# Kernel optimization log

Measured on AMD Instinct MI355X. Metric: run time of the kernel, lower is better.

The kernel has to match this reference:

```python
import jax, jax.numpy as jnp
import numpy as np
from jax import lax


def _make_grid():
    # Faithful replication of the torch buffer construction in __init__.
    r = np.arange(-128, 128) * np.pi / 256.0
    X, Y = np.meshgrid(r, r, indexing='ij')            # torch.meshgrid default 'ij'
    grid = np.tile(np.stack([X, Y], 0), (16, 1, 1))    # [32,256,256] channels x,y,x,y,...
    scales = 2.0 ** np.repeat(np.arange(16) / 2.0, 2)  # [32]: f0,f0,f1,f1,...
    grid = np.sin(grid * scales[:, None, None])
    return jnp.asarray(grid.reshape(32, 256 * 256).T, dtype=jnp.float32)  # [65536,32]

IMG_GRID = _make_grid()


def _conv_lrelu(x, w, b, padding, groups):
    y = lax.conv_general_dilated(x, w, (1, 1), padding,
                                 feature_group_count=groups,
                                 dimension_numbers=('NCHW', 'OIHW', 'NCHW'))
    return jax.nn.leaky_relu(y + b[None, :, None, None])


def _wn_linear(x, v, g, b):
    # nn.utils.weight_norm(Linear): w = g * v / ||v||  (norm over input dim, per output row)
    w = v * (g / jnp.linalg.norm(v, axis=1))[:, None]
    return x @ w.T + b


def _mem_stack(x, vf, gf, bf, vg, gg, bg):
    # memcnn AdditiveCoupling: x1,x2 = chunk(x,2); y1 = x1 + Fm(x2); y2 = x2 + Gm(y1)
    def step(h, p):
        pvf, pgf, pbf, pvg, pgg, pbg = p
        h1, h2 = jnp.split(h, 2, axis=-1)
        y1 = h1 + jax.nn.leaky_relu(_wn_linear(h2, pvf, pgf, pbf))
        y2 = h2 + jax.nn.leaky_relu(_wn_linear(y1, pvg, pgg, pbg))
        return jnp.concatenate([y1, y2], axis=-1), None
    h, _ = lax.scan(step, x, (vf, gf, bf, vg, gg, bg))
    return h


def _forward(feature, cw1, cb1, cw2, cb2, cw3, cb3, cw4, cb4, cw5, cb5,
             w1, b1, m1_vf, m1_gf, m1_bf, m1_vg, m1_gg, m1_bg,
             w2, b2, m2_vf, m2_gf, m2_bf, m2_vg, m2_gg, m2_bg, w3, b3):
    B = feature.shape[0]
    h = _conv_lrelu(feature, cw1, cb1, 'SAME', 4)
    h = _conv_lrelu(h, cw2, cb2, 'SAME', 3)
    h = _conv_lrelu(h, cw3, cb3, 'SAME', 2)
    h = _conv_lrelu(h, cw4, cb4, 'VALID', 3)
    h = _conv_lrelu(h, cw5, cb5, 'VALID', 1)   # [B,128,4,4]
    feat = h.reshape(B, -1)                    # [B,2048]
    N = IMG_GRID.shape[0]                      # 65536 coords, fully vectorized (no python chunk loop)
    grid_b = jnp.broadcast_to(IMG_GRID[None], (B, N, 32))
    x = jnp.concatenate([grid_b, jnp.broadcast_to(feat[:, None, :], (B, N, feat.shape[1]))], -1)
    mid = jax.nn.leaky_relu(x @ w1.T + b1)     # [B,N,1024]
    mid = _mem_stack(mid, m1_vf, m1_gf, m1_bf, m1_vg, m1_gg, m1_bg)
    h2 = jax.nn.leaky_relu(jnp.concatenate([grid_b, mid], -1) @ w2.T + b2)  # [B,N,512]
    h2 = _mem_stack(h2, m2_vf, m2_gf, m2_bf, m2_vg, m2_gg, m2_bg)
    rgb = jax.nn.sigmoid(h2 @ w3.T + b3)       # [B,N,3]
    img = rgb.transpose(0, 2, 1).reshape(B, 3, 256, 256)
    return img * 1.1 - 0.05


def setup_inputs() -> dict:
    key = jax.random.key(0)
    ks = iter(jax.random.split(key, 48))
    def nrm(shape, s=0.02):
        return jax.random.normal(next(ks), shape, jnp.float32) * s
    def gpar(shape):
        return jax.random.uniform(next(ks), shape, jnp.float32, 0.5, 1.0)
    inp = {}
    inp['feature'] = jax.random.normal(next(ks), (1, 1792, 8, 8), jnp.float32)
    inp['cw1'] = nrm((768, 448, 3, 3)); inp['cb1'] = nrm((768,), 0.01)   # groups=4: 1792/4=448
    inp['cw2'] = nrm((768, 256, 3, 3)); inp['cb2'] = nrm((768,), 0.01)   # groups=3
    inp['cw3'] = nrm((768, 384, 3, 3)); inp['cb3'] = nrm((768,), 0.01)   # groups=2
    inp['cw4'] = nrm((768, 256, 3, 3)); inp['cb4'] = nrm((768,), 0.01)   # groups=3, valid
    inp['cw5'] = nrm((128, 768, 3, 3)); inp['cb5'] = nrm((128,), 0.01)   # groups=1, valid
    inp['w1'] = nrm((1024, 2080)); inp['b1'] = nrm((1024,), 0.01)
    inp['m1_vf'] = nrm((8, 512, 512), 1.0); inp['m1_gf'] = gpar((8, 512)); inp['m1_bf'] = nrm((8, 512), 0.01)
    inp['m1_vg'] = nrm((8, 512, 512), 1.0); inp['m1_gg'] = gpar((8, 512)); inp['m1_bg'] = nrm((8, 512), 0.01)
    inp['w2'] = nrm((512, 1056)); inp['b2'] = nrm((512,), 0.01)
    inp['m2_vf'] = nrm((8, 256, 256), 1.0); inp['m2_gf'] = gpar((8, 256)); inp['m2_bf'] = nrm((8, 256), 0.01)
    inp['m2_vg'] = nrm((8, 256, 256), 1.0); inp['m2_gg'] = gpar((8, 256)); inp['m2_bg'] = nrm((8, 256), 0.01)
    inp['w3'] = nrm((3, 512)); inp['b3'] = nrm((3,), 0.01)
    return inp


def reference(feature, cw1, cb1, cw2, cb2, cw3, cb3, cw4, cb4, cw5, cb5,
              w1, b1, m1_vf, m1_gf, m1_bf, m1_vg, m1_gg, m1_bg,
              w2, b2, m2_vf, m2_gf, m2_bf, m2_vg, m2_gg, m2_bg, w3, b3):
    return _forward(feature, cw1, cb1, cw2, cb2, cw3, cb3, cw4, cb4, cw5, cb5,
                    w1, b1, m1_vf, m1_gf, m1_bf, m1_vg, m1_gg, m1_bg,
                    w2, b2, m2_vf, m2_gf, m2_bf, m2_vg, m2_gg, m2_bg, w3, b3)
```

## Files before the change

### kernel.cpp

```cpp
#include <hip/hip_runtime.h>
#include <cmath>

#define LRELU(x) fmaxf((x), 0.01f * (x))

typedef __attribute__((ext_vector_type(8))) short short8;
typedef __attribute__((ext_vector_type(4))) float f32x4;
typedef __attribute__((ext_vector_type(2))) unsigned uint2v;

constexpr int RS = 1032;

__device__ __forceinline__ unsigned short f2bf(float f) {
    return __builtin_bit_cast(unsigned short, (__bf16)f);
}
__device__ __forceinline__ unsigned pk2(unsigned short a, unsigned short b) {
    return (unsigned)a | ((unsigned)b << 16);
}
__device__ __forceinline__ uint2v cvt4(f32x4 v) {
    uint2v r;
    r[0] = pk2(f2bf(v[0]), f2bf(v[1]));
    r[1] = pk2(f2bf(v[2]), f2bf(v[3]));
    return r;
}
__device__ __forceinline__ f32x4 unpk4(uint2v p) {
    f32x4 r;
    r[0] = __uint_as_float(p[0] << 16);
    r[1] = __uint_as_float(p[0] & 0xffff0000u);
    r[2] = __uint_as_float(p[1] << 16);
    r[3] = __uint_as_float(p[1] & 0xffff0000u);
    return r;
}
__device__ __forceinline__ f32x4 lrelu4(f32x4 v) {
    return __builtin_elementwise_max(v, 0.01f * v);
}

__global__ void sgrid_kernel(float* __restrict__ sg) {
    int idx = blockIdx.x * blockDim.x + threadIdx.x;
    if (idx >= 256 * 32) return;
    int t = idx >> 5, c = idx & 31;
    double r = (double)(t - 128) * 3.14159265358979323846 / 256.0;
    double scale = exp2(0.5 * (double)(c >> 1));
    sg[idx] = (float)sin(r * scale);
}

__global__ __launch_bounds__(256) void conv_part(
    const float* __restrict__ x, const float* __restrict__ w,
    float* __restrict__ y, int Cin_g, int Cout_g, int Hin, int pad) {
    __shared__ float wsh[64 * 9];
    __shared__ float red[256];
    int oc = blockIdx.x, ch = blockIdx.y;
    int Hout = pad ? Hin : Hin - 2;
    int t = threadIdx.x;
    int ic0 = ch * 64;
    int nic = min(64, Cin_g - ic0);
    const float* wb = w + ((size_t)oc * Cin_g + ic0) * 9;
    for (int i = t; i < nic * 9; i += 256) wsh[i] = wb[i];
    __syncthreads();
    int p = t & 63, sub = t >> 6;
    int oy = p / Hout, ox = p % Hout;
    int g = oc / Cout_g;
    const float* xb = x + ((size_t)g * Cin_g + ic0) * Hin * Hin;
    bool valid = p < Hout * Hout;
    float acc = 0.f;
    if (valid) {
        for (int ic = sub; ic < nic; ic += 4) {
            const float* xc = xb + (size_t)ic * Hin * Hin;
            const float* wc = wsh + ic * 9;
            #pragma unroll
            for (int ky = 0; ky < 3; ++ky) {
                int iy = oy + ky - pad;
                if (iy < 0 || iy >= Hin) continue;
                #pragma unroll
                for (int kx = 0; kx < 3; ++kx) {
                    int ix = ox + kx - pad;
                    if (ix < 0 || ix >= Hin) continue;
                    acc = fmaf(xc[iy * Hin + ix], wc[ky * 3 + kx], acc);
                }
            }
        }
    }
    red[t] = acc;
    __syncthreads();
    if (t < 64 && valid)
        atomicAdd(&y[(size_t)oc * Hout * Hout + p],
                  red[t] + red[t + 64] + red[t + 128] + red[t + 192]);
}

__global__ void conv_finalize(float* __restrict__ y, const float* __restrict__ bias,
                              int HH, int n) {
    int i = blockIdx.x * 256 + threadIdx.x;
    if (i >= n) return;
    float v = y[i] + bias[i / HH];
    y[i] = LRELU(v);
}

__global__ void feat_c1_kernel(const float* __restrict__ feat, const float* __restrict__ w1,
                               const float* __restrict__ b1, float* __restrict__ c1) {
    int o = (blockIdx.x * blockDim.x + threadIdx.x) >> 6;
    int lane = threadIdx.x & 63;
    if (o >= 1024) return;
    const float* wr = w1 + (size_t)o * 2080 + 32;
    float sum = 0.f;
    for (int k = lane; k < 2048; k += 64) sum += feat[k] * wr[k];
    #pragma unroll
    for (int off = 32; off; off >>= 1) sum += __shfl_xor(sum, off);
    if (lane == 0) c1[o] = sum + b1[o];
}

__global__ __launch_bounds__(256) void wn_all(
    const float* __restrict__ v1f, const float* __restrict__ g1f, float* __restrict__ s1f,
    const float* __restrict__ v1g, const float* __restrict__ g1g, float* __restrict__ s1g,
    const float* __restrict__ v2f, const float* __restrict__ g2f, float* __restrict__ s2f,
    const float* __restrict__ v2g, const float* __restrict__ g2g, float* __restrict__ s2g) {
    __shared__ float red[256];
    int b = blockIdx.x, t = threadIdx.x;
    const float* v; const float* g; float* s; int K, r;
    if (b < 4096)       { v = v1f; g = g1f; s = s1f; K = 512; r = b; }
    else if (b < 8192)  { v = v1g; g = g1g; s = s1g; K = 512; r = b - 4096; }
    else if (b < 10240) { v = v2f; g = g2f; s = s2f; K = 256; r = b - 8192; }
    else                { v = v2g; g = g2g; s = s2g; K = 256; r = b - 10240; }
    const float* vr = v + (size_t)r * K;
    float sum = 0.f;
    for (int k = t; k < K; k += 256) { float x = vr[k]; sum = fmaf(x, x, sum); }
    red[t] = sum;
    __syncthreads();
    for (int o = 128; o; o >>= 1) {
        if (t < o) red[t] += red[t + o];
        __syncthreads();
    }
    if (t == 0) s[r] = g[r] / sqrtf(red[0]);
}

__device__ __forceinline__ void repack_one(const float* __restrict__ v, unsigned short* __restrict__ dst,
                                           int N, int NT, int KC, int ldk, int koff, size_t fi) {
    int W = N / (NT * 16);
    int l = (int)(fi & 63);
    size_t r = fi >> 6;
    int kc = r % KC; r /= KC;
    int nt = r % NT; r /= NT;
    int w  = r % W;  r /= W;
    int t  = (int)r;
    int n = w * NT * 16 + nt * 16 + (l & 15);
    int k = kc * 32 + (l >> 4) * 8;
    const float* src = v + ((size_t)t * N + n) * ldk + koff + k;
    unsigned short* d = dst + fi * 8;
    #pragma unroll
    for (int e = 0; e < 8; ++e) d[e] = f2bf(src[e]);
}

__global__ void repack_all(const float* __restrict__ m1vf, const float* __restrict__ m1vg,
                           const float* __restrict__ m2vf, const float* __restrict__ m2vg,
                           const float* __restrict__ w2,
                           unsigned short* __restrict__ p1f, unsigned short* __restrict__ p1g,
                           unsigned short* __restrict__ p2f, unsigned short* __restrict__ p2g,
                           unsigned short* __restrict__ pw2) {
    size_t fi = (size_t)blockIdx.x * 256 + threadIdx.x;
    const size_t n1 = 262144, n2 = 65536;
    if (fi < n1)                repack_one(m1vf, p1f, 512, 4, 16, 512, 0, fi);
    else if (fi < 2 * n1)       repack_one(m1vg, p1g, 512, 4, 16, 512, 0, fi - n1);
    else if (fi < 2 * n1 + n2)  repack_one(m2vf, p2f, 256, 2, 8, 256, 0, fi - 2 * n1);
    else if (fi < 2 * n1 + 2 * n2) repack_one(m2vg, p2g, 256, 2, 8, 256, 0, fi - 2 * n1 - n2);
    else                        repack_one(w2, pw2, 512, 4, 32, 1056, 32, fi - 2 * n1 - 2 * n2);
}

__global__ void pq_kernel(const float* __restrict__ sg, const float* __restrict__ w1,
                          const float* __restrict__ c1, const float* __restrict__ w2,
                          float* __restrict__ Px, float* __restrict__ Py,
                          float* __restrict__ Qx, float* __restrict__ Qy) {
    int idx = blockIdx.x * 256 + threadIdx.x;
    if (idx < 256 * 1024) {
        int t = idx >> 10, o = idx & 1023;
        const float* wr = w1 + (size_t)o * 2080;
        const float* sr = sg + t * 32;
        float px = 0.f, py = 0.f;
        #pragma unroll
        for (int k = 0; k < 16; ++k) {
            px = fmaf(sr[2 * k], wr[2 * k], px);
            py = fmaf(sr[2 * k + 1], wr[2 * k + 1], py);
        }
        Px[idx] = px + c1[o];
        Py[idx] = py;
    } else {
        int j = idx - 256 * 1024;
        int t = j >> 9, o = j & 511;
        const float* wr = w2 + (size_t)o * 1056;
        const float* sr = sg + t * 32;
        float qx = 0.f, qy = 0.f;
        #pragma unroll
        for (int k = 0; k < 16; ++k) {
            qx = fmaf(sr[2 * k], wr[2 * k], qx);
            qy = fmaf(sr[2 * k + 1], wr[2 * k + 1], qy);
        }
        Qx[j] = qx;
        Qy[j] = qy;
    }
}

__device__ __forceinline__ void step1(unsigned short* sm, int w, int l, int l15, int lq,
                                      int srcb, int dstb,
                                      const unsigned short* __restrict__ Bp,
                                      const float* __restrict__ sc,
                                      const float* __restrict__ bi,
                                      uint2v* lo_half) {
    f32x4 acc[4][4] = {};
    const unsigned short* wb = Bp + (size_t)w * (4 * 16 * 512) + (size_t)l * 8;
    const unsigned short* abase = sm + (size_t)l15 * RS + srcb + lq * 8;
    short8 b0[4], b1[4];
    #pragma unroll
    for (int nt = 0; nt < 4; ++nt) b0[nt] = *(const short8*)(wb + (size_t)(nt * 16 + 0) * 512);
    #pragma unroll
    for (int nt = 0; nt < 4; ++nt) b1[nt] = *(const short8*)(wb + (size_t)(nt * 16 + 1) * 512);
    #pragma unroll
    for (int kc = 0; kc < 16; ++kc) {
        short8 bn[4];
        if (kc < 14) {
            #pragma unroll
            for (int nt = 0; nt < 4; ++nt)
                bn[nt] = *(const short8*)(wb + (size_t)(nt * 16 + kc + 2) * 512);
        }
        short8 af[4];
        #pragma unroll
        for (int mt = 0; mt < 4; ++mt)
            af[mt] = *(const short8*)(abase + (size_t)(mt * 16) * RS + kc * 32);
        #pragma unroll
        for (int mt = 0; mt < 4; ++mt)
            #pragma unroll
            for (int nt = 0; nt < 4; ++nt)
                acc[mt][nt] = __builtin_amdgcn_mfma_f32_16x16x32_bf16(b0[nt], af[mt], acc[mt][nt], 0, 0, 0);
        #pragma unroll
        for (int nt = 0; nt < 4; ++nt) { b0[nt] = b1[nt]; b1[nt] = bn[nt]; }
    }
    #pragma unroll
    for (int nt = 0; nt < 4; ++nt) {
        int nb = w * 64 + nt * 16 + lq * 4;
        f32x4 s4 = *(const f32x4*)(sc + nb);
        f32x4 bb = *(const f32x4*)(bi + nb);
        #pragma unroll
        for (int mt = 0; mt < 4; ++mt) {
            int row = mt * 16 + l15;
            size_t hidx = (size_t)row * RS + dstb + nb;
            uint2v hold = *(uint2v*)(sm + hidx);
            f32x4 v = lrelu4(acc[mt][nt] * s4 + bb);
            v += unpk4(hold) + unpk4(lo_half[mt * 4 + nt]);
            uint2v hnew = cvt4(v);
            *(uint2v*)(sm + hidx) = hnew;
            lo_half[mt * 4 + nt] = cvt4(v - unpk4(hnew));
        }
    }
}

__device__ __forceinline__ void step2(unsigned short* sm, int w, int l, int l15, int lq,
                                      int srcb, int dstb,
                                      const unsigned short* __restrict__ Bp,
                                      const float* __restrict__ sc,
                                      const float* __restrict__ bi) {
    f32x4 acc[4][2] = {};
    const unsigned short* wb = Bp + (size_t)w * (2 * 8 * 512) + (size_t)l * 8;
    const unsigned short* abase = sm + (size_t)l15 * RS + srcb + lq * 8;
    short8 b0[2], b1[2];
    #pragma unroll
    for (int nt = 0; nt < 2; ++nt) b0[nt] = *(const short8*)(wb + (size_t)(nt * 8 + 0) * 512);
    #pragma unroll
    for (int nt = 0; nt < 2; ++nt) b1[nt] = *(const short8*)(wb + (size_t)(nt * 8 + 1) * 512);
    #pragma unroll
    for (int kc = 0; kc < 8; ++kc) {
        short8 bn[2];
        if (kc < 6) {
            #pragma unroll
            for (int nt = 0; nt < 2; ++nt)
                bn[nt] = *(const short8*)(wb + (size_t)(nt * 8 + kc + 2) * 512);
        }
        short8 af[4];
        #pragma unroll
        for (int mt = 0; mt < 4; ++mt)
            af[mt] = *(const short8*)(abase + (size_t)(mt * 16) * RS + kc * 32);
        #pragma unroll
        for (int mt = 0; mt < 4; ++mt)
            #pragma unroll
            for (int nt = 0; nt < 2; ++nt)
                acc[mt][nt] = __builtin_amdgcn_mfma_f32_16x16x32_bf16(b0[nt], af[mt], acc[mt][nt], 0, 0, 0);
        #pragma unroll
        for (int nt = 0; nt < 2; ++nt) { b0[nt] = b1[nt]; b1[nt] = bn[nt]; }
    }
    #pragma unroll
    for (int nt = 0; nt < 2; ++nt) {
        int nb = w * 32 + nt * 16 + lq * 4;
        f32x4 s4 = *(const f32x4*)(sc + nb);
        f32x4 bb = *(const f32x4*)(bi + nb);
        #pragma unroll
        for (int mt = 0; mt < 4; ++mt) {
            int row = mt * 16 + l15;
            size_t hidx = (size_t)row * RS + dstb + nb;
            uint2v hold = *(uint2v*)(sm + hidx);
            uint2v lold = *(uint2v*)(sm + hidx + 512);
            f32x4 v = lrelu4(acc[mt][nt] * s4 + bb);
            v += unpk4(hold) + unpk4(lold);
            uint2v hnew = cvt4(v);
            *(uint2v*)(sm + hidx) = hnew;
            *(uint2v*)(sm + hidx + 512) = cvt4(v - unpk4(hnew));
        }
    }
}

__global__ __launch_bounds__(512, 2) void fused_mlp(
    const float* __restrict__ Px, const float* __restrict__ Py,
    const float* __restrict__ Qx, const float* __restrict__ Qy,
    const unsigned short* __restrict__ m1f, const float* __restrict__ s1f, const float* __restrict__ bf1,
    const unsigned short* __restrict__ m1g, const float* __restrict__ s1g, const float* __restrict__ bg1,
    const unsigned short* __restrict__ w2m, const float* __restrict__ b2,
    const unsigned short* __restrict__ m2f, const float* __restrict__ s2f, const float* __restrict__ bf2_,
    const unsigned short* __restrict__ m2g, const float* __restrict__ s2g, const float* __restrict__ bg2_,
    const float* __restrict__ w3, const float* __restrict__ b3,
    float* __restrict__ out) {
    extern __shared__ unsigned short sm[];
    int tid = threadIdx.x;
    int w = tid >> 6, l = tid & 63;
    int l15 = l & 15, lq = l >> 4;
    int n0 = blockIdx.x * 64;
    int i = n0 >> 8, jb = n0 & 255;

    uint2v lo_pk[32];

    #pragma unroll
    for (int h = 0; h < 2; ++h) {
        #pragma unroll
        for (int nt = 0; nt < 4; ++nt) {
            int nb = h * 512 + w * 64 + nt * 16 + lq * 4;
            f32x4 px4 = *(const f32x4*)(Px + (size_t)i * 1024 + nb);
            #pragma unroll
            for (int mt = 0; mt < 4; ++mt) {
                int row = mt * 16 + l15;
                f32x4 py4 = *(const f32x4*)(Py + (size_t)(jb + row) * 1024 + nb);
                f32x4 v = lrelu4(px4 + py4);
                uint2v hv = cvt4(v);
                *(uint2v*)(sm + (size_t)row * RS + nb) = hv;
                lo_pk[h * 16 + mt * 4 + nt] = cvt4(v - unpk4(hv));
            }
        }
    }
    __syncthreads();

    for (int t = 0; t < 8; ++t) {
        step1(sm, w, l, l15, lq, 512, 0, m1f + (size_t)t * 512 * 512, s1f + t * 512, bf1 + t * 512, lo_pk);
        __syncthreads();
        step1(sm, w, l, l15, lq, 0, 512, m1g + (size_t)t * 512 * 512, s1g + t * 512, bg1 + t * 512, lo_pk + 16);
        __syncthreads();
    }

    {
        f32x4 acc[4][4] = {};
        const unsigned short* wb = w2m + (size_t)w * (4 * 32 * 512) + (size_t)l * 8;
        const unsigned short* abase = sm + (size_t)l15 * RS + lq * 8;
        short8 b0[4], b1[4];
        #pragma unroll
        for (int nt = 0; nt < 4; ++nt) b0[nt] = *(const short8*)(wb + (size_t)(nt * 32 + 0) * 512);
        #pragma unroll
        for (int nt = 0; nt < 4; ++nt) b1[nt] = *(const short8*)(wb + (size_t)(nt * 32 + 1) * 512);
        #pragma unroll
        for (int kc = 0; kc < 32; ++kc) {
            short8 bn[4];
            if (kc < 30) {
                #pragma unroll
                for (int nt = 0; nt < 4; ++nt)
                    bn[nt] = *(const short8*)(wb + (size_t)(nt * 32 + kc + 2) * 512);
            }
            short8 af[4];
            #pragma unroll
            for (int mt = 0; mt < 4; ++mt)
                af[mt] = *(const short8*)(abase + (size_t)(mt * 16) * RS + kc * 32);
            #pragma unroll
            for (int mt = 0; mt < 4; ++mt)
                #pragma unroll
                for (int nt = 0; nt < 4; ++nt)
                    acc[mt][nt] = __builtin_amdgcn_mfma_f32_16x16x32_bf16(b0[nt], af[mt], acc[mt][nt], 0, 0, 0);
            #pragma unroll
            for (int nt = 0; nt < 4; ++nt) { b0[nt] = b1[nt]; b1[nt] = bn[nt]; }
        }
        __syncthreads();
        #pragma unroll
        for (int nt = 0; nt < 4; ++nt) {
            int nb = w * 64 + nt * 16 + lq * 4;
            f32x4 qx4 = *(const f32x4*)(Qx + (size_t)i * 512 + nb);
            f32x4 b24 = *(const f32x4*)(b2 + nb);
            #pragma unroll
            for (int mt = 0; mt < 4; ++mt) {
                int row = mt * 16 + l15;
                f32x4 qy4 = *(const f32x4*)(Qy + (size_t)(jb + row) * 512 + nb);
                f32x4 v = lrelu4(acc[mt][nt] + qx4 + qy4 + b24);
                uint2v hv = cvt4(v);
                size_t hidx = (size_t)row * RS + nb;
                *(uint2v*)(sm + hidx) = hv;
                *(uint2v*)(sm + hidx + 512) = cvt4(v - unpk4(hv));
            }
        }
    }
    __syncthreads();

    for (int t = 0; t < 8; ++t) {
        step2(sm, w, l, l15, lq, 256, 0, m2f + (size_t)t * 256 * 256, s2f + t * 256, bf2_ + t * 256);
        __syncthreads();
        step2(sm, w, l, l15, lq, 0, 256, m2g + (size_t)t * 256 * 256, s2g + t * 256, bg2_ + t * 256);
        __syncthreads();
    }

    #pragma unroll
    for (int rr = 0; rr < 8; ++rr) {
        int row = w * 8 + rr;
        float s0 = 0.f, s1 = 0.f, s2 = 0.f;
        #pragma unroll
        for (int it = 0; it < 8; ++it) {
            int k = it * 64 + l;
            size_t hidx = (size_t)row * RS + k;
            float hv = __uint_as_float((unsigned)sm[hidx] << 16) +
                       __uint_as_float((unsigned)sm[hidx + 512] << 16);
            s0 = fmaf(hv, w3[k], s0);
            s1 = fmaf(hv, w3[512 + k], s1);
            s2 = fmaf(hv, w3[1024 + k], s2);
        }
        #pragma unroll
        for (int off = 32; off; off >>= 1) {
            s0 += __shfl_xor(s0, off);
            s1 += __shfl_xor(s1, off);
            s2 += __shfl_xor(s2, off);
        }
        if (l == 0) {
            float v[3] = {s0 + b3[0], s1 + b3[1], s2 + b3[2]};
            #pragma unroll
            for (int c = 0; c < 3; ++c) {
                float sg = 1.0f / (1.0f + expf(-v[c]));
                out[(size_t)c * 65536 + n0 + row] = 1.1f * sg - 0.05f;
            }
        }
    }
}

extern "C" void kernel_launch(void* const* d_in, const int* in_sizes, int n_in,
                              void* d_out, int out_size, void* d_ws, size_t ws_size,
                              hipStream_t stream) {
    const float* feature = (const float*)d_in[0];
    const float* cw1 = (const float*)d_in[1];  const float* cb1 = (const float*)d_in[2];
    const float* cw2 = (const float*)d_in[3];  const float* cb2 = (const float*)d_in[4];
    const float* cw3 = (const float*)d_in[5];  const float* cb3 = (const float*)d_in[6];
    const float* cw4 = (const float*)d_in[7];  const float* cb4 = (const float*)d_in[8];
    const float* cw5 = (const float*)d_in[9];  const float* cb5 = (const float*)d_in[10];
    const float* w1  = (const float*)d_in[11]; const float* b1  = (const float*)d_in[12];
    const float* m1_vf = (const float*)d_in[13]; const float* m1_gf = (const float*)d_in[14];
    const float* m1_bf = (const float*)d_in[15];
    const float* m1_vg = (const float*)d_in[16]; const float* m1_gg = (const float*)d_in[17];
    const float* m1_bg = (const float*)d_in[18];
    const float* w2  = (const float*)d_in[19]; const float* b2  = (const float*)d_in[20];
    const float* m2_vf = (const float*)d_in[21]; const float* m2_gf = (const float*)d_in[22];
    const float* m2_bf = (const float*)d_in[23];
    const float* m2_vg = (const float*)d_in[24]; const float* m2_gg = (const float*)d_in[25];
    const float* m2_bg = (const float*)d_in[26];
    const float* w3  = (const float*)d_in[27]; const float* b3  = (const float*)d_in[28];
    float* out = (float*)d_out;

    float* ws = (float*)d_ws;
    size_t off = 0;
    float* sgrid   = ws + off; off += 256 * 32;
    float* cbA     = ws + off; off += 768 * 64;
    float* cbB     = ws + off; off += 768 * 64;
    float* cbC     = ws + off; off += 768 * 64;
    float* cbD     = ws + off; off += 768 * 36;
    float* featbuf = ws + off; off += 2048;
    size_t convN   = 768 * 64 * 3 + 768 * 36 + 2048;
    float* c1      = ws + off; off += 1024;
    float* s1f     = ws + off; off += 8 * 512;
    float* s1g     = ws + off; off += 8 * 512;
    float* s2f     = ws + off; off += 8 * 256;
    float* s2g     = ws + off; off += 8 * 256;
    float* Px      = ws + off; off += 256 * 1024;
    float* Py      = ws + off; off += 256 * 1024;
    float* Qx      = ws + off; off += 256 * 512;
    float* Qy      = ws + off; off += 256 * 512;
    unsigned short* m1f_p = (unsigned short*)(ws + off); off += (size_t)8 * 512 * 512 / 2;
    unsigned short* m1g_p = (unsigned short*)(ws + off); off += (size_t)8 * 512 * 512 / 2;
    unsigned short* m2f_p = (unsigned short*)(ws + off); off += (size_t)8 * 256 * 256 / 2;
    unsigned short* m2g_p = (unsigned short*)(ws + off); off += (size_t)8 * 256 * 256 / 2;
    unsigned short* w2m_p = (unsigned short*)(ws + off); off += (size_t)512 * 1024 / 2;

    sgrid_kernel<<<32, 256, 0, stream>>>(sgrid);
    wn_all<<<12288, 256, 0, stream>>>(m1_vf, m1_gf, s1f, m1_vg, m1_gg, s1g,
                                      m2_vf, m2_gf, s2f, m2_vg, m2_gg, s2g);
    repack_all<<<2816, 256, 0, stream>>>(m1_vf, m1_vg, m2_vf, m2_vg, w2,
                                         m1f_p, m1g_p, m2f_p, m2g_p, w2m_p);

    hipMemsetAsync(cbA, 0, convN * sizeof(float), stream);
    conv_part<<<dim3(768, 7), 256, 0, stream>>>(feature, cw1, cbA, 448, 192, 8, 1);
    conv_finalize<<<(768 * 64) / 256, 256, 0, stream>>>(cbA, cb1, 64, 768 * 64);
    conv_part<<<dim3(768, 4), 256, 0, stream>>>(cbA, cw2, cbB, 256, 256, 8, 1);
    conv_finalize<<<(768 * 64) / 256, 256, 0, stream>>>(cbB, cb2, 64, 768 * 64);
    conv_part<<<dim3(768, 6), 256, 0, stream>>>(cbB, cw3, cbC, 384, 384, 8, 1);
    conv_finalize<<<(768 * 64) / 256, 256, 0, stream>>>(cbC, cb3, 64, 768 * 64);
    conv_part<<<dim3(768, 4), 256, 0, stream>>>(cbC, cw4, cbD, 256, 256, 8, 0);
    conv_finalize<<<(768 * 36 + 255) / 256, 256, 0, stream>>>(cbD, cb4, 36, 768 * 36);
    conv_part<<<dim3(128, 12), 256, 0, stream>>>(cbD, cw5, featbuf, 768, 128, 6, 0);
    conv_finalize<<<(2048 + 255) / 256, 256, 0, stream>>>(featbuf, cb5, 16, 2048);

    feat_c1_kernel<<<1024 / 4, 256, 0, stream>>>(featbuf, w1, b1, c1);
    pq_kernel<<<(256 * 1024 + 256 * 512) / 256, 256, 0, stream>>>(sgrid, w1, c1, w2, Px, Py, Qx, Qy);

    size_t lds_bytes = (size_t)64 * RS * sizeof(unsigned short);
    hipFuncSetAttribute(reinterpret_cast<const void*>(fused_mlp),
                        hipFuncAttributeMaxDynamicSharedMemorySize, (int)lds_bytes);
    fused_mlp<<<1024, 512, lds_bytes, stream>>>(
        Px, Py, Qx, Qy,
        m1f_p, s1f, m1_bf, m1g_p, s1g, m1_bg,
        w2m_p, b2,
        m2f_p, s2f, m2_bf, m2g_p, s2g, m2_bg,
        w3, b3, out);
}
```

Measured before the change: 1.282 ms.

## Halve rows per block in fused MLP to raise occupancy, shorten weight prefetch

The fused MLP kernel now handles 32 coordinate rows per block instead of 64, which halves LDS use and accumulator registers and doubles the grid to 2048 blocks. Launch bounds go from 2 to 4 blocks per CU. The weight prefetch pipeline shrinks from double-ahead to single-ahead buffering to save registers. The trade-off is that each weight fragment is reused across only half as many rows, so global/L2 weight traffic per output doubles. Hiding load latency now relies on having more waves resident.

```diff
diff --git a/kernel.cpp b/kernel.cpp
--- a/kernel.cpp
+++ b/kernel.cpp
@@ -8,6 +8,7 @@
 typedef __attribute__((ext_vector_type(2))) unsigned uint2v;
 
 constexpr int RS = 1032;
+constexpr int ROWS = 32;
 
 __device__ __forceinline__ unsigned short f2bf(float f) {
     return __builtin_bit_cast(unsigned short, (__bf16)f);
@@ -201,33 +202,31 @@
                                       const float* __restrict__ sc,
                                       const float* __restrict__ bi,
                                       uint2v* lo_half) {
-    f32x4 acc[4][4] = {};
+    f32x4 acc[2][4] = {};
     const unsigned short* wb = Bp + (size_t)w * (4 * 16 * 512) + (size_t)l * 8;
     const unsigned short* abase = sm + (size_t)l15 * RS + srcb + lq * 8;
-    short8 b0[4], b1[4];
-    #pragma unroll
-    for (int nt = 0; nt < 4; ++nt) b0[nt] = *(const short8*)(wb + (size_t)(nt * 16 + 0) * 512);
-    #pragma unroll
-    for (int nt = 0; nt < 4; ++nt) b1[nt] = *(const short8*)(wb + (size_t)(nt * 16 + 1) * 512);
+    short8 bcur[4];
+    #pragma unroll
+    for (int nt = 0; nt < 4; ++nt) bcur[nt] = *(const short8*)(wb + (size_t)(nt * 16) * 512);
     #pragma unroll
     for (int kc = 0; kc < 16; ++kc) {
         short8 bn[4];
-        if (kc < 14) {
+        if (kc < 15) {
             #pragma unroll
             for (int nt = 0; nt < 4; ++nt)
-                bn[nt] = *(const short8*)(wb + (size_t)(nt * 16 + kc + 2) * 512);
-        }
-        short8 af[4];
-        #pragma unroll
-        for (int mt = 0; mt < 4; ++mt)
+                bn[nt] = *(const short8*)(wb + (size_t)(nt * 16 + kc + 1) * 512);
+        }
+        short8 af[2];
+        #pragma unroll
+        for (int mt = 0; mt < 2; ++mt)
             af[mt] = *(const short8*)(abase + (size_t)(mt * 16) * RS + kc * 32);
         #pragma unroll
-        for (int mt = 0; mt < 4; ++mt)
+        for (int mt = 0; mt < 2; ++mt)
             #pragma unroll
             for (int nt = 0; nt < 4; ++nt)
-                acc[mt][nt] = __builtin_amdgcn_mfma_f32_16x16x32_bf16(b0[nt], af[mt], acc[mt][nt], 0, 0, 0);
-        #pragma unroll
-        for (int nt = 0; nt < 4; ++nt) { b0[nt] = b1[nt]; b1[nt] = bn[nt]; }
+                acc[mt][nt] = __builtin_amdgcn_mfma_f32_16x16x32_bf16(bcur[nt], af[mt], acc[mt][nt], 0, 0, 0);
+        #pragma unroll
+        for (int nt = 0; nt < 4; ++nt) bcur[nt] = bn[nt];
     }
     #pragma unroll
     for (int nt = 0; nt < 4; ++nt) {
@@ -235,7 +234,7 @@
         f32x4 s4 = *(const f32x4*)(sc + nb);
         f32x4 bb = *(const f32x4*)(bi + nb);
         #pragma unroll
-        for (int mt = 0; mt < 4; ++mt) {
+        for (int mt = 0; mt < 2; ++mt) {
             int row = mt * 16 + l15;
             size_t hidx = (size_t)row * RS + dstb + nb;
             uint2v hold = *(uint2v*)(sm + hidx);
@@ -253,33 +252,31 @@
                                       const unsigned short* __restrict__ Bp,
                                       const float* __restrict__ sc,
                                       const float* __restrict__ bi) {
-    f32x4 acc[4][2] = {};
+    f32x4 acc[2][2] = {};
     const unsigned short* wb = Bp + (size_t)w * (2 * 8 * 512) + (size_t)l * 8;
     const unsigned short* abase = sm + (size_t)l15 * RS + srcb + lq * 8;
-    short8 b0[2], b1[2];
-    #pragma unroll
-    for (int nt = 0; nt < 2; ++nt) b0[nt] = *(const short8*)(wb + (size_t)(nt * 8 + 0) * 512);
-    #pragma unroll
-    for (int nt = 0; nt < 2; ++nt) b1[nt] = *(const short8*)(wb + (size_t)(nt * 8 + 1) * 512);
+    short8 bcur[2];
+    #pragma unroll
+    for (int nt = 0; nt < 2; ++nt) bcur[nt] = *(const short8*)(wb + (size_t)(nt * 8) * 512);
     #pragma unroll
     for (int kc = 0; kc < 8; ++kc) {
         short8 bn[2];
-        if (kc < 6) {
+        if (kc < 7) {
             #pragma unroll
             for (int nt = 0; nt < 2; ++nt)
-                bn[nt] = *(const short8*)(wb + (size_t)(nt * 8 + kc + 2) * 512);
-        }
-        short8 af[4];
-        #pragma unroll
-        for (int mt = 0; mt < 4; ++mt)
+                bn[nt] = *(const short8*)(wb + (size_t)(nt * 8 + kc + 1) * 512);
+        }
+        short8 af[2];
+        #pragma unroll
+        for (int mt = 0; mt < 2; ++mt)
             af[mt] = *(const short8*)(abase + (size_t)(mt * 16) * RS + kc * 32);
         #pragma unroll
-        for (int mt = 0; mt < 4; ++mt)
+        for (int mt = 0; mt < 2; ++mt)
             #pragma unroll
             for (int nt = 0; nt < 2; ++nt)
-                acc[mt][nt] = __builtin_amdgcn_mfma_f32_16x16x32_bf16(b0[nt], af[mt], acc[mt][nt], 0, 0, 0);
-        #pragma unroll
-        for (int nt = 0; nt < 2; ++nt) { b0[nt] = b1[nt]; b1[nt] = bn[nt]; }
+                acc[mt][nt] = __builtin_amdgcn_mfma_f32_16x16x32_bf16(bcur[nt], af[mt], acc[mt][nt], 0, 0, 0);
+        #pragma unroll
+        for (int nt = 0; nt < 2; ++nt) bcur[nt] = bn[nt];
     }
     #pragma unroll
     for (int nt = 0; nt < 2; ++nt) {
@@ -287,7 +284,7 @@
         f32x4 s4 = *(const f32x4*)(sc + nb);
         f32x4 bb = *(const f32x4*)(bi + nb);
         #pragma unroll
-        for (int mt = 0; mt < 4; ++mt) {
+        for (int mt = 0; mt < 2; ++mt) {
             int row = mt * 16 + l15;
             size_t hidx = (size_t)row * RS + dstb + nb;
             uint2v hold = *(uint2v*)(sm + hidx);
@@ -301,7 +298,7 @@
     }
 }
 
-__global__ __launch_bounds__(512, 2) void fused_mlp(
+__global__ __launch_bounds__(512, 4) void fused_mlp(
     const float* __restrict__ Px, const float* __restrict__ Py,
     const float* __restrict__ Qx, const float* __restrict__ Qy,
     const unsigned short* __restrict__ m1f, const float* __restrict__ s1f, const float* __restrict__ bf1,
@@ -315,10 +312,10 @@
     int tid = threadIdx.x;
     int w = tid >> 6, l = tid & 63;
     int l15 = l & 15, lq = l >> 4;
-    int n0 = blockIdx.x * 64;
+    int n0 = blockIdx.x * ROWS;
     int i = n0 >> 8, jb = n0 & 255;
 
-    uint2v lo_pk[32];
+    uint2v lo_pk[16];
 
     #pragma unroll
     for (int h = 0; h < 2; ++h) {
@@ -327,13 +324,13 @@
             int nb = h * 512 + w * 64 + nt * 16 + lq * 4;
             f32x4 px4 = *(const f32x4*)(Px + (size_t)i * 1024 + nb);
             #pragma unroll
-            for (int mt = 0; mt < 4; ++mt) {
+            for (int mt = 0; mt < 2; ++mt) {
                 int row = mt * 16 + l15;
                 f32x4 py4 = *(const f32x4*)(Py + (size_t)(jb + row) * 1024 + nb);
                 f32x4 v = lrelu4(px4 + py4);
                 uint2v hv = cvt4(v);
                 *(uint2v*)(sm + (size_t)row * RS + nb) = hv;
-                lo_pk[h * 16 + mt * 4 + nt] = cvt4(v - unpk4(hv));
+                lo_pk[h * 8 + mt * 4 + nt] = cvt4(v - unpk4(hv));
             }
         }
     }
@@ -342,38 +339,36 @@
     for (int t = 0; t < 8; ++t) {
         step1(sm, w, l, l15, lq, 512, 0, m1f + (size_t)t * 512 * 512, s1f + t * 512, bf1 + t * 512, lo_pk);
         __syncthreads();
-        step1(sm, w, l, l15, lq, 0, 512, m1g + (size_t)t * 512 * 512, s1g + t * 512, bg1 + t * 512, lo_pk + 16);
+        step1(sm, w, l, l15, lq, 0, 512, m1g + (size_t)t * 512 * 512, s1g + t * 512, bg1 + t * 512, lo_pk + 8);
         __syncthreads();
     }
 
     {
-        f32x4 acc[4][4] = {};
+        f32x4 acc[2][4] = {};
         const unsigned short* wb = w2m + (size_t)w * (4 * 32 * 512) + (size_t)l * 8;
         const unsigned short* abase = sm + (size_t)l15 * RS + lq * 8;
-        short8 b0[4], b1[4];
-        #pragma unroll
-        for (int nt = 0; nt < 4; ++nt) b0[nt] = *(const short8*)(wb + (size_t)(nt * 32 + 0) * 512);
-        #pragma unroll
-        for (int nt = 0; nt < 4; ++nt) b1[nt] = *(const short8*)(wb + (size_t)(nt * 32 + 1) * 512);
+        short8 bcur[4];
+        #pragma unroll
+        for (int nt = 0; nt < 4; ++nt) bcur[nt] = *(const short8*)(wb + (size_t)(nt * 32) * 512);
         #pragma unroll
         for (int kc = 0; kc < 32; ++kc) {
             short8 bn[4];
-            if (kc < 30) {
+            if (kc < 31) {
                 #pragma unroll
                 for (int nt = 0; nt < 4; ++nt)
-                    bn[nt] = *(const short8*)(wb + (size_t)(nt * 32 + kc + 2) * 512);
+                    bn[nt] = *(const short8*)(wb + (size_t)(nt * 32 + kc + 1) * 512);
             }
-            short8 af[4];
-            #pragma unroll
-            for (int mt = 0; mt < 4; ++mt)
+            short8 af[2];
+            #pragma unroll
+            for (int mt = 0; mt < 2; ++mt)
                 af[mt] = *(const short8*)(abase + (size_t)(mt * 16) * RS + kc * 32);
             #pragma unroll
-            for (int mt = 0; mt < 4; ++mt)
+            for (int mt = 0; mt < 2; ++mt)
                 #pragma unroll
                 for (int nt = 0; nt < 4; ++nt)
-                    acc[mt][nt] = __builtin_amdgcn_mfma_f32_16x16x32_bf16(b0[nt], af[mt], acc[mt][nt], 0, 0, 0);
-            #pragma unroll
-            for (int nt = 0; nt < 4; ++nt) { b0[nt] = b1[nt]; b1[nt] = bn[nt]; }
+                    acc[mt][nt] = __builtin_amdgcn_mfma_f32_16x16x32_bf16(bcur[nt], af[mt], acc[mt][nt], 0, 0, 0);
+            #pragma unroll
+            for (int nt = 0; nt < 4; ++nt) bcur[nt] = bn[nt];
         }
         __syncthreads();
         #pragma unroll
@@ -382,7 +377,7 @@
             f32x4 qx4 = *(const f32x4*)(Qx + (size_t)i * 512 + nb);
             f32x4 b24 = *(const f32x4*)(b2 + nb);
             #pragma unroll
-            for (int mt = 0; mt < 4; ++mt) {
+            for (int mt = 0; mt < 2; ++mt) {
                 int row = mt * 16 + l15;
                 f32x4 qy4 = *(const f32x4*)(Qy + (size_t)(jb + row) * 512 + nb);
                 f32x4 v = lrelu4(acc[mt][nt] + qx4 + qy4 + b24);
@@ -403,8 +398,8 @@
     }
 
     #pragma unroll
-    for (int rr = 0; rr < 8; ++rr) {
-        int row = w * 8 + rr;
+    for (int rr = 0; rr < 4; ++rr) {
+        int row = w * 4 + rr;
         float s0 = 0.f, s1 = 0.f, s2 = 0.f;
         #pragma unroll
         for (int it = 0; it < 8; ++it) {
@@ -500,10 +495,10 @@
     feat_c1_kernel<<<1024 / 4, 256, 0, stream>>>(featbuf, w1, b1, c1);
     pq_kernel<<<(256 * 1024 + 256 * 512) / 256, 256, 0, stream>>>(sgrid, w1, c1, w2, Px, Py, Qx, Qy);
 
-    size_t lds_bytes = (size_t)64 * RS * sizeof(unsigned short);
+    size_t lds_bytes = (size_t)ROWS * RS * sizeof(unsigned short);
     hipFuncSetAttribute(reinterpret_cast<const void*>(fused_mlp),
                         hipFuncAttributeMaxDynamicSharedMemorySize, (int)lds_bytes);
-    fused_mlp<<<1024, 512, lds_bytes, stream>>>(
+    fused_mlp<<<65536 / ROWS, 512, lds_bytes, stream>>>(
         Px, Py, Qx, Qy,
         m1f_p, s1f, m1_bf, m1g_p, s1g, m1_bg,
         w2m_p, b2,
```

Measured after the change: 1.533 ms. +19.6%, slower.
